# Kernel tuning notes

Hardware: AMD Instinct MI355X
Metric: run time of the kernel (lower is better)

Reference implementation:

```python
import jax, jax.numpy as jnp
import numpy as np

GROUP_SIZE = 32
OUT_FEATURES = 4096
IN_FEATURES = 4096


def _unpack_3bit(p):
    # p: [..., 3] uint8 -> [..., 8] 3-bit values in [0, 7]
    b0, b1, b2 = p[..., 0], p[..., 1], p[..., 2]
    v0 = b0 & 7
    v1 = (b0 >> 3) & 7
    v2 = ((b0 >> 6) & 3) | ((b1 & 1) << 2)
    v3 = (b1 >> 1) & 7
    v4 = (b1 >> 4) & 7
    v5 = ((b1 >> 7) & 1) | ((b2 & 3) << 1)
    v6 = (b2 >> 2) & 7
    v7 = (b2 >> 5) & 7
    return jnp.stack([v0, v1, v2, v3, v4, v5, v6, v7], axis=-1)


def _block_dequantize_3bit(packed, normalization, group_size=GROUP_SIZE):
    # packed: [n_groups, group_size*3//8] int8, normalization: [n_groups, 1]
    p = packed.astype(jnp.uint8).reshape(-1, group_size // 8, 3)
    q = _unpack_3bit(p).reshape(-1, group_size).astype(jnp.float32)
    n = normalization.astype(jnp.float32)  # [n_groups, 1]
    x_norm = q / 7.0
    return (x_norm * (2.0 * n) - n).reshape(-1)


def setup_inputs() -> dict:
    key = jax.random.key(0)
    k1, k2, k3, k4 = jax.random.split(key, 4)
    n_groups = OUT_FEATURES * IN_FEATURES // GROUP_SIZE
    packed_cols = GROUP_SIZE * 3 // 8
    x = jax.random.normal(k1, (2, 2048, IN_FEATURES), dtype=jnp.float32)
    weight_q3 = jax.random.randint(k2, (n_groups, packed_cols), 0, 256, dtype=jnp.int32).astype(jnp.int8)
    weight_norm = jax.random.uniform(k3, (n_groups, 1), dtype=jnp.float32, minval=0.05, maxval=1.0)
    bias = jax.random.normal(k4, (OUT_FEATURES,), dtype=jnp.float32) * 0.02
    return {"x": x, "weight_q3": weight_q3, "weight_norm": weight_norm, "bias": bias}


def reference(x, weight_q3, weight_norm, bias):
    # Dequantize 3-bit packed weights to fp32 [out, in], then F.linear.
    w = _block_dequantize_3bit(weight_q3, weight_norm).reshape(OUT_FEATURES, IN_FEATURES)
    return jnp.einsum('bsi,oi->bso', x, w) + bias
```

## Files before the change

kernel.cpp:

```cpp
#include <hip/hip_runtime.h>
#include <hip/hip_bf16.h>
#include <stdint.h>

#define OUTF 4096
#define INF  4096
#define MROWS 4096
#define GS 32

typedef __attribute__((ext_vector_type(8))) __bf16 bf16x8;
typedef __attribute__((ext_vector_type(4))) float f32x4;

__device__ inline void gload_lds16(const void* g, void* l) {
    __builtin_amdgcn_global_load_lds(
        (const __attribute__((address_space(1))) void*)g,
        (__attribute__((address_space(3))) void*)l, 16, 0, 0);
}

__device__ inline void load_group_bits(const int* __restrict__ wq, int gid,
                                       uint64_t& lo, uint64_t& hi) {
    const int4* p = (const int4*)(wq + (size_t)gid * 12);
    int4 A = p[0], B = p[1], C = p[2];
    uint32_t d0 = (uint32_t)(A.x & 255) | ((uint32_t)(A.y & 255) << 8) |
                  ((uint32_t)(A.z & 255) << 16) | ((uint32_t)(A.w & 255) << 24);
    uint32_t d1 = (uint32_t)(B.x & 255) | ((uint32_t)(B.y & 255) << 8) |
                  ((uint32_t)(B.z & 255) << 16) | ((uint32_t)(B.w & 255) << 24);
    uint32_t d2 = (uint32_t)(C.x & 255) | ((uint32_t)(C.y & 255) << 8) |
                  ((uint32_t)(C.z & 255) << 16) | ((uint32_t)(C.w & 255) << 24);
    lo = (uint64_t)d0 | ((uint64_t)d1 << 32);
    hi = (uint64_t)d1 | ((uint64_t)d2 << 32);
}

__global__ void prep_kernel(const float* __restrict__ x, __bf16* __restrict__ xb,
                            const int* __restrict__ wq, const float* __restrict__ wn,
                            __bf16* __restrict__ wb) {
    const int bid = blockIdx.x;
    if (bid < 8192) {
        int i = bid * 256 + threadIdx.x;
        const f32x4* xp = (const f32x4*)x;
        f32x4 a = xp[2 * i], b = xp[2 * i + 1];
        bf16x8 v = { (__bf16)a[0], (__bf16)a[1], (__bf16)a[2], (__bf16)a[3],
                     (__bf16)b[0], (__bf16)b[1], (__bf16)b[2], (__bf16)b[3] };
        ((bf16x8*)xb)[i] = v;
    } else {
        int gid = (bid - 8192) * 256 + threadIdx.x;
        uint64_t lo, hi;
        load_group_bits(wq, gid, lo, hi);
        float nrm = wn[gid];
        float c2 = nrm * (2.0f / 7.0f), c1 = -nrm;
        bf16x8 o[4];
#pragma unroll
        for (int j = 0; j < 32; ++j) {
            uint32_t q = (j <= 20) ? (uint32_t)((lo >> (3 * j)) & 7)
                                   : (uint32_t)((hi >> (3 * j - 32)) & 7);
            o[j >> 3][j & 7] = (__bf16)((float)q * c2 + c1);
        }
        bf16x8* outp = (bf16x8*)(wb + (size_t)gid * 32);
        outp[0] = o[0]; outp[1] = o[1]; outp[2] = o[2]; outp[3] = o[3];
    }
}


#define RD_A(DST, RB, H) do { \
    _Pragma("unroll") \
    for (int m_ = 0; m_ < 4; ++m_) { \
        const int r_ = wr * 64 + m_ * 16 + row16; \
        _Pragma("unroll") \
        for (int kk_ = 0; kk_ < 2; ++kk_) \
            DST[m_][kk_] = *(const bf16x8*)(lds + (RB) * 65536 + (H) * 16384 + \
                r_ * 128 + (((kk_ * 4 + kq) * 16) ^ ((r_ & 7) << 4))); \
    } \
} while (0)

#define RD_B(DST, RB, H) do { \
    _Pragma("unroll") \
    for (int n_ = 0; n_ < 2; ++n_) { \
        const int r_ = wc * 32 + n_ * 16 + row16; \
        _Pragma("unroll") \
        for (int kk_ = 0; kk_ < 2; ++kk_) \
            DST[n_][kk_] = *(const bf16x8*)(lds + (RB) * 65536 + 32768 + (H) * 16384 + \
                r_ * 128 + (((kk_ * 4 + kq) * 16) ^ ((r_ & 7) << 4))); \
    } \
} while (0)

#define STAGE(SB, AB, H, SKT) do { \
    const __bf16* base_ = (AB) ? wb : xb; \
    const int brc_ = ((AB) ? bn : bm) * 256; \
    _Pragma("unroll") \
    for (int j_ = 0; j_ < 2; ++j_) \
        gload_lds16((const char*)(base_ + (size_t)(brc_ + (H) * 128 + j_ * 64 + srow) * INF + \
                                  (SKT) * 64 + schunk * 8), \
                    lds + (SB) * 65536 + (AB) * 32768 + (H) * 16384 + j_ * 8192 + tid * 16); \
} while (0)

#define MF_Q(A_, B_, MH, NH) do { \
    __builtin_amdgcn_s_setprio(1); \
    _Pragma("unroll") \
    for (int kk_ = 0; kk_ < 2; ++kk_) \
        _Pragma("unroll") \
        for (int m_ = 0; m_ < 4; ++m_) \
            _Pragma("unroll") \
            for (int n_ = 0; n_ < 2; ++n_) \
                acc[MH][NH][m_][n_] = __builtin_amdgcn_mfma_f32_16x16x32_bf16( \
                    A_[m_][kk_], B_[n_][kk_], acc[MH][NH][m_][n_], 0, 0, 0); \
    __builtin_amdgcn_s_setprio(0); \
} while (0)

__global__ __launch_bounds__(512, 2) void gemm8_kernel(
    const __bf16* __restrict__ xb, const __bf16* __restrict__ wb,
    const float* __restrict__ bias, float* __restrict__ out) {
    __shared__ __align__(16) unsigned char lds[131072];

    const int tid = threadIdx.x;
    const int lane = tid & 63, wid = tid >> 6;
    const int wr = wid >> 2, wc = wid & 3;
    const int row16 = lane & 15, kq = lane >> 4;

    const int bid = blockIdx.x;
    const int wg = (bid & 7) * 32 + (bid >> 3);
    const int bn = wg & 15, bm = wg >> 4;

    const int srow = tid >> 3;
    const int schunk = (tid & 7) ^ (srow & 7);

    f32x4 acc[2][2][4][2] = {};
    bf16x8 a[4][2], b0[2][2], b1[2][2];

    STAGE(0, 0, 0, 0); STAGE(0, 1, 0, 0); STAGE(0, 0, 1, 0); STAGE(0, 1, 1, 0);
    __syncthreads();
    RD_A(a, 0, 0); RD_B(b0, 0, 0);

    for (int kt = 0; kt < INF / 64; ++kt) {
        const int rb = kt & 1, sb = rb ^ 1, nt = (kt + 1) & 63;
        STAGE(sb, 0, 0, nt); STAGE(sb, 1, 0, nt);
        STAGE(sb, 0, 1, nt); STAGE(sb, 1, 1, nt);
        RD_B(b1, rb, 1);
        MF_Q(a, b0, 0, 0);
        MF_Q(a, b1, 0, 1);
        RD_A(a, rb, 1);
        MF_Q(a, b1, 1, 1);
        MF_Q(a, b0, 1, 0);
        __syncthreads();
        RD_A(a, sb, 0); RD_B(b0, sb, 0);
    }

#pragma unroll
    for (int nh = 0; nh < 2; ++nh)
#pragma unroll
        for (int n = 0; n < 2; ++n) {
            const int col = bn * 256 + nh * 128 + wc * 32 + n * 16 + row16;
            const float bv = bias[col];
#pragma unroll
            for (int mh = 0; mh < 2; ++mh)
#pragma unroll
                for (int m = 0; m < 4; ++m) {
                    const int rbase = bm * 256 + mh * 128 + wr * 64 + m * 16 + kq * 4;
#pragma unroll
                    for (int j = 0; j < 4; ++j)
                        out[(size_t)(rbase + j) * OUTF + col] = acc[mh][nh][m][n][j] + bv;
                }
        }
}

__global__ __launch_bounds__(256, 2) void gemm_fb_kernel(
    const float* __restrict__ x, const int* __restrict__ wq,
    const float* __restrict__ wn, const float* __restrict__ bias,
    float* __restrict__ out) {
    __shared__ __align__(16) unsigned char lAraw[128 * 128];
    __shared__ __align__(16) unsigned char lBraw[128 * 128];

    const int tid = threadIdx.x;
    const int lane = tid & 63, wid = tid >> 6;
    const int wr = wid >> 1, wc = wid & 1;
    const int bn = blockIdx.x, bm = blockIdx.y;
    const int row16 = lane & 15, kq = lane >> 4;

    f32x4 acc[4][4] = {};

    int aoff[4], boff[4];
#pragma unroll
    for (int m = 0; m < 4; ++m) {
        int r = wr * 64 + m * 16 + row16;
        aoff[m] = r * 128 + ((kq * 16) ^ ((r & 7) << 4));
    }
#pragma unroll
    for (int n = 0; n < 4; ++n) {
        int r = wc * 64 + n * 16 + row16;
        boff[n] = r * 128 + ((kq * 16) ^ ((r & 7) << 4));
    }

    for (int kt = 0; kt < INF / 64; ++kt) {
        __syncthreads();
#pragma unroll
        for (int it = 0; it < 4; ++it) {
            int row = it * 32 + (tid >> 3), c = tid & 7;
            const f32x4* xp = (const f32x4*)(x + (size_t)(bm * 128 + row) * INF + kt * 64 + c * 8);
            f32x4 a0 = xp[0], a1 = xp[1];
            bf16x8 v = { (__bf16)a0[0], (__bf16)a0[1], (__bf16)a0[2], (__bf16)a0[3],
                         (__bf16)a1[0], (__bf16)a1[1], (__bf16)a1[2], (__bf16)a1[3] };
            *(bf16x8*)(lAraw + row * 128 + ((c * 16) ^ ((row & 7) << 4))) = v;
        }
        {
            int row = tid >> 1, gi = tid & 1;
            int gid = (bn * 128 + row) * (INF / GS) + kt * 2 + gi;
            uint64_t lo, hi;
            load_group_bits(wq, gid, lo, hi);
            float nrm = wn[gid];
            float c2 = nrm * (2.0f / 7.0f), c1 = -nrm;
            bf16x8 o[4];
#pragma unroll
            for (int j = 0; j < 32; ++j) {
                uint32_t q = (j <= 20) ? (uint32_t)((lo >> (3 * j)) & 7)
                                       : (uint32_t)((hi >> (3 * j - 32)) & 7);
                o[j >> 3][j & 7] = (__bf16)((float)q * c2 + c1);
            }
            unsigned swz = (row & 7) << 4;
#pragma unroll
            for (int c4 = 0; c4 < 4; ++c4)
                *(bf16x8*)(lBraw + row * 128 + ((gi * 64 + c4 * 16) ^ swz)) = o[c4];
        }
        __syncthreads();

#pragma unroll
        for (int kk = 0; kk < 2; ++kk) {
            bf16x8 afr[4], bfr[4];
#pragma unroll
            for (int m = 0; m < 4; ++m)
                afr[m] = *(const bf16x8*)(lAraw + (aoff[m] ^ (kk * 64)));
#pragma unroll
            for (int n = 0; n < 4; ++n)
                bfr[n] = *(const bf16x8*)(lBraw + (boff[n] ^ (kk * 64)));
#pragma unroll
            for (int m = 0; m < 4; ++m)
#pragma unroll
                for (int n = 0; n < 4; ++n)
                    acc[m][n] = __builtin_amdgcn_mfma_f32_16x16x32_bf16(afr[m], bfr[n], acc[m][n], 0, 0, 0);
        }
    }

#pragma unroll
    for (int n = 0; n < 4; ++n) {
        int col = bn * 128 + wc * 64 + n * 16 + row16;
        float bv = bias[col];
#pragma unroll
        for (int m = 0; m < 4; ++m) {
            int rbase = bm * 128 + wr * 64 + m * 16 + kq * 4;
#pragma unroll
            for (int j = 0; j < 4; ++j)
                out[(size_t)(rbase + j) * OUTF + col] = acc[m][n][j] + bv;
        }
    }
}

extern "C" void kernel_launch(void* const* d_in, const int* in_sizes, int n_in,
                              void* d_out, int out_size, void* d_ws, size_t ws_size,
                              hipStream_t stream) {
    const float* x    = (const float*)d_in[0];
    const int*   wq   = (const int*)d_in[1];
    const float* wn   = (const float*)d_in[2];
    const float* bias = (const float*)d_in[3];
    float* out = (float*)d_out;

    const size_t xb_bytes = (size_t)MROWS * INF * 2;
    const size_t wb_bytes = (size_t)OUTF * INF * 2;
    if (ws_size >= xb_bytes + wb_bytes) {
        __bf16* xb = (__bf16*)d_ws;
        __bf16* wb = (__bf16*)((char*)d_ws + xb_bytes);
        prep_kernel<<<8192 + (OUTF * INF / GS) / 256, 256, 0, stream>>>(x, xb, wq, wn, wb);
        gemm8_kernel<<<(MROWS / 256) * (OUTF / 256), 512, 0, stream>>>(xb, wb, bias, out);
    } else {
        gemm_fb_kernel<<<dim3(OUTF / 128, MROWS / 128), 256, 0, stream>>>(x, wq, wn, bias, out);
    }
}
```

Baseline: 145.8 us.

## Restructure GEMM main loop into fine-grained 8-wave ping-pong schedule with explicit waitcnt

The GEMM main loop is rewritten so that each 64-wide K tile is split into four quarter-phases. Global-to-LDS loads for later tiles (up to two ahead) are interleaved with LDS reads and MFMA quarters, using explicit vmcnt/lgkmcnt waits and raw s_barrier instead of a single __syncthreads per iteration. The aim is to overlap memory traffic with MFMA work more tightly and to cut full-barrier stalls. The prep kernel is also split into separate x-conversion and weight-dequant launches, which adds one extra kernel launch. The hand-tuned wait counts are fragile: the initial prologue stages only three quarters of buffer 1 and relies on the loop to stage the rest, so any miscount could cause races.

```diff
diff --git a/kernel.cpp b/kernel.cpp
--- a/kernel.cpp
+++ b/kernel.cpp
@@ -30,35 +30,40 @@
     hi = (uint64_t)d1 | ((uint64_t)d2 << 32);
 }
 
-__global__ void prep_kernel(const float* __restrict__ x, __bf16* __restrict__ xb,
-                            const int* __restrict__ wq, const float* __restrict__ wn,
-                            __bf16* __restrict__ wb) {
-    const int bid = blockIdx.x;
-    if (bid < 8192) {
-        int i = bid * 256 + threadIdx.x;
-        const f32x4* xp = (const f32x4*)x;
-        f32x4 a = xp[2 * i], b = xp[2 * i + 1];
-        bf16x8 v = { (__bf16)a[0], (__bf16)a[1], (__bf16)a[2], (__bf16)a[3],
-                     (__bf16)b[0], (__bf16)b[1], (__bf16)b[2], (__bf16)b[3] };
-        ((bf16x8*)xb)[i] = v;
-    } else {
-        int gid = (bid - 8192) * 256 + threadIdx.x;
-        uint64_t lo, hi;
-        load_group_bits(wq, gid, lo, hi);
-        float nrm = wn[gid];
-        float c2 = nrm * (2.0f / 7.0f), c1 = -nrm;
-        bf16x8 o[4];
-#pragma unroll
-        for (int j = 0; j < 32; ++j) {
-            uint32_t q = (j <= 20) ? (uint32_t)((lo >> (3 * j)) & 7)
-                                   : (uint32_t)((hi >> (3 * j - 32)) & 7);
-            o[j >> 3][j & 7] = (__bf16)((float)q * c2 + c1);
-        }
-        bf16x8* outp = (bf16x8*)(wb + (size_t)gid * 32);
-        outp[0] = o[0]; outp[1] = o[1]; outp[2] = o[2]; outp[3] = o[3];
-    }
-}
-
+__global__ void cvt_x_kernel(const float* __restrict__ x, __bf16* __restrict__ xb, int n8) {
+    int i = blockIdx.x * blockDim.x + threadIdx.x;
+    if (i >= n8) return;
+    const f32x4* xp = (const f32x4*)x;
+    f32x4 a = xp[2 * i], b = xp[2 * i + 1];
+    bf16x8 v = { (__bf16)a[0], (__bf16)a[1], (__bf16)a[2], (__bf16)a[3],
+                 (__bf16)b[0], (__bf16)b[1], (__bf16)b[2], (__bf16)b[3] };
+    ((bf16x8*)xb)[i] = v;
+}
+
+__global__ void dequant_w_kernel(const int* __restrict__ wq,
+                                 const float* __restrict__ wn,
+                                 __bf16* __restrict__ wb) {
+    int gid = blockIdx.x * blockDim.x + threadIdx.x;
+    uint64_t lo, hi;
+    load_group_bits(wq, gid, lo, hi);
+    float nrm = wn[gid];
+    float c2 = nrm * (2.0f / 7.0f), c1 = -nrm;
+    bf16x8 o[4];
+#pragma unroll
+    for (int j = 0; j < 32; ++j) {
+        uint32_t q = (j <= 20) ? (uint32_t)((lo >> (3 * j)) & 7)
+                               : (uint32_t)((hi >> (3 * j - 32)) & 7);
+        o[j >> 3][j & 7] = (__bf16)((float)q * c2 + c1);
+    }
+    bf16x8* outp = (bf16x8*)(wb + (size_t)gid * 32);
+    outp[0] = o[0]; outp[1] = o[1]; outp[2] = o[2]; outp[3] = o[3];
+}
+
+
+#define VMCNT(N) asm volatile("s_waitcnt vmcnt(" #N ")" ::: "memory")
+#define LGKM(N)  asm volatile("s_waitcnt lgkmcnt(" #N ")" ::: "memory")
+#define BARR() do { asm volatile("" ::: "memory"); __builtin_amdgcn_s_barrier(); \
+                    asm volatile("" ::: "memory"); } while (0)
 
 #define RD_A(DST, RB, H) do { \
     _Pragma("unroll") \
@@ -105,6 +110,17 @@
     __builtin_amdgcn_s_setprio(0); \
 } while (0)
 
+#define TILE(RB, T) do { \
+    RD_A(af, RB, 0); RD_B(bP, RB, 0); STAGE((RB) ^ 1, 1, 0, ((T) + 1) & 63); \
+        LGKM(8); BARR(); MF_Q(af, bP, 0, 0); BARR(); \
+    RD_B(bQ, RB, 1); STAGE(RB, 0, 0, ((T) + 2) & 63); \
+        BARR(); MF_Q(af, bQ, 0, 1); BARR(); \
+    RD_A(af, RB, 1); STAGE(RB, 1, 1, ((T) + 2) & 63); \
+        BARR(); MF_Q(af, bQ, 1, 1); BARR(); \
+    STAGE(RB, 0, 1, ((T) + 2) & 63); \
+        VMCNT(6); BARR(); MF_Q(af, bP, 1, 0); BARR(); \
+} while (0)
+
 __global__ __launch_bounds__(512, 2) void gemm8_kernel(
     const __bf16* __restrict__ xb, const __bf16* __restrict__ wb,
     const float* __restrict__ bias, float* __restrict__ out) {
@@ -123,24 +139,16 @@
     const int schunk = (tid & 7) ^ (srow & 7);
 
     f32x4 acc[2][2][4][2] = {};
-    bf16x8 a[4][2], b0[2][2], b1[2][2];
-
-    STAGE(0, 0, 0, 0); STAGE(0, 1, 0, 0); STAGE(0, 0, 1, 0); STAGE(0, 1, 1, 0);
-    __syncthreads();
-    RD_A(a, 0, 0); RD_B(b0, 0, 0);
-
-    for (int kt = 0; kt < INF / 64; ++kt) {
-        const int rb = kt & 1, sb = rb ^ 1, nt = (kt + 1) & 63;
-        STAGE(sb, 0, 0, nt); STAGE(sb, 1, 0, nt);
-        STAGE(sb, 0, 1, nt); STAGE(sb, 1, 1, nt);
-        RD_B(b1, rb, 1);
-        MF_Q(a, b0, 0, 0);
-        MF_Q(a, b1, 0, 1);
-        RD_A(a, rb, 1);
-        MF_Q(a, b1, 1, 1);
-        MF_Q(a, b0, 1, 0);
-        __syncthreads();
-        RD_A(a, sb, 0); RD_B(b0, sb, 0);
+    bf16x8 af[4][2], bP[2][2], bQ[2][2];
+
+    STAGE(0, 0, 0, 0); STAGE(0, 1, 0, 0); STAGE(0, 1, 1, 0); STAGE(0, 0, 1, 0);
+    STAGE(1, 0, 0, 1); STAGE(1, 1, 1, 1); STAGE(1, 0, 1, 1);
+    VMCNT(6);
+    BARR();
+
+    for (int kt = 0; kt < INF / 64; kt += 2) {
+        TILE(0, kt);
+        TILE(1, kt + 1);
     }
 
 #pragma unroll
@@ -265,7 +273,8 @@
     if (ws_size >= xb_bytes + wb_bytes) {
         __bf16* xb = (__bf16*)d_ws;
         __bf16* wb = (__bf16*)((char*)d_ws + xb_bytes);
-        prep_kernel<<<8192 + (OUTF * INF / GS) / 256, 256, 0, stream>>>(x, xb, wq, wn, wb);
+        cvt_x_kernel<<<(MROWS * INF / 8 + 255) / 256, 256, 0, stream>>>(x, xb, MROWS * INF / 8);
+        dequant_w_kernel<<<(OUTF * INF / GS) / 256, 256, 0, stream>>>(wq, wn, wb);
         gemm8_kernel<<<(MROWS / 256) * (OUTF / 256), 512, 0, stream>>>(xb, wb, bias, out);
     } else {
         gemm_fb_kernel<<<dim3(OUTF / 128, MROWS / 128), 256, 0, stream>>>(x, wq, wn, bias, out);
```

Measured after the change: 148.9 us. 2.1% more time.
